# Kernel tuning notes

Hardware: AMD Instinct MI355X
Metric: run time of the kernel (lower is better)

## Reference

```python
import jax, jax.numpy as jnp
import numpy as np

N = 4096        # nodes
D = 512         # in_dim = hidden_dim
E = 131072      # edges (avg degree 32)
K = 3           # aggregate_range
ALPHA = 2.0


def prelu(x, a):
    return jnp.where(x >= 0, x, a * x)


def setup_inputs() -> dict:
    key = jax.random.key(0)
    ks = jax.random.split(key, 8)
    s = 1.0 / np.sqrt(D)  # ~xavier scale
    return {
        "coeffs": jax.random.normal(ks[0], (N, D), jnp.float32),
        "edge_index": jax.random.randint(ks[1], (2, E), 0, N, dtype=jnp.int32),
        "W0": jax.random.normal(ks[2], (D, D), jnp.float32) * s,
        "b0": jnp.zeros((D,), jnp.float32),
        "a0": jnp.full((1,), 0.25, jnp.float32),
        "W1": jax.random.normal(ks[3], (D, D), jnp.float32) * s,  # use_bias=False
        "a1": jnp.full((1,), 0.25, jnp.float32),
        "W2": jax.random.normal(ks[4], (D, D), jnp.float32) * s,
        "a2": jnp.full((1,), 0.25, jnp.float32),
        "Wo": jax.random.normal(ks[5], (1, D), jnp.float32) * s,
        "bo": jnp.zeros((1,), jnp.float32),
    }


def _mlp(coeffs, W0, b0, a0, W1, a1, W2, a2, Wo, bo):
    # Linear+PReLU, then n_hidden_layers x [Linear(no bias)+PReLU+(Dropout: eval, no-op)], then Linear
    x = prelu(coeffs @ W0.T + b0, a0)
    x = prelu(x @ W1.T, a1)
    x = prelu(x @ W2.T, a2)
    return x @ Wo.T + bo  # [N, 1]


def _aggregate_k_hop(edge_index, angles):
    # Faithful to the torch code: enhanced_angles aliases angles, so each hop
    # reads the CURRENT (already enhanced) values:  a <- a + w_k * A_k @ a.
    # Hop 1 uses raw edge list (duplicate edges add twice). Hops >= 2 use
    # np.unique-deduplicated composed paths == boolean adjacency powers.
    src, dst = edge_index[0], edge_index[1]
    a = angles
    a = a + (0.5 ** ALPHA) * jax.ops.segment_sum(a[dst], src, num_segments=N)
    A = jnp.zeros((N, N), jnp.float32).at[src, dst].set(1.0)  # dedup'd boolean adjacency
    Ak = A
    for k_ in range(K - 1):
        Ak = ((Ak @ A) > 0).astype(jnp.float32)  # unique k-hop paths
        a = a + (1.0 / (k_ + 3)) ** ALPHA * (Ak @ a)
    return a


def reference(coeffs, edge_index, W0, b0, a0, W1, a1, W2, a2, Wo, bo):
    angles = _mlp(coeffs, W0, b0, a0, W1, a1, W2, a2, Wo, bo)
    return _aggregate_k_hop(edge_index, angles)
```

## Files before the change

kernel.cpp:

```cpp
#include <hip/hip_runtime.h>

#define N_NODES 4096
#define D_DIM   512
#define E_EDGES 131072
#define NWORDS  128

typedef __bf16 bf16;
typedef __bf16 bf16x4 __attribute__((ext_vector_type(4)));
typedef __bf16 bf16x8 __attribute__((ext_vector_type(8)));
typedef float  f32x4  __attribute__((ext_vector_type(4)));
typedef unsigned int u32;

#define GLOAD_LDS16(gp, lp) \
    __builtin_amdgcn_global_load_lds((const __attribute__((address_space(1))) u32*)(gp), \
                                     (__attribute__((address_space(3))) u32*)(lp), 16, 0, 0)

static const size_t OFF_W0B = 0;
static const size_t OFF_W1B = OFF_W0B + (size_t)D_DIM*D_DIM*2;
static const size_t OFF_W2B = OFF_W1B + (size_t)D_DIM*D_DIM*2;
static const size_t OFF_X0  = OFF_W2B + (size_t)D_DIM*D_DIM*2;
static const size_t OFF_X1  = OFF_X0  + (size_t)N_NODES*D_DIM*2;
static const size_t OFF_X2  = OFF_X1  + (size_t)N_NODES*D_DIM*2;
static const size_t OFF_ANG = OFF_X2  + (size_t)N_NODES*D_DIM*2;
static const size_t OFF_H1  = OFF_ANG + N_NODES*4;
static const size_t OFF_A2V = OFF_H1  + N_NODES*4;
static const size_t OFF_TP  = OFF_A2V + N_NODES*4;
static const size_t OFF_AB  = OFF_TP  + 1024*4;
static const size_t OFF_A2B = OFF_AB  + (size_t)N_NODES*NWORDS*4;
static const size_t OFF_A3B = OFF_A2B + (size_t)N_NODES*NWORDS*4;

__global__ __launch_bounds__(256)
void prep(const float* __restrict__ coeffs, const float* __restrict__ W0,
          const float* __restrict__ W1, const float* __restrict__ W2,
          const float* __restrict__ bo,
          bf16* __restrict__ x0b, bf16* __restrict__ W0b,
          bf16* __restrict__ W1b, bf16* __restrict__ W2b,
          u32* __restrict__ Ab, float* __restrict__ ang, float* __restrict__ h1)
{
    const int bx = blockIdx.x, t = threadIdx.x;
    if (bx < 512) {
        const float* src = coeffs + (size_t)bx * 4096;
        bf16* dst = x0b + (size_t)bx * 4096;
        #pragma unroll
        for (int i = 0; i < 4; ++i) {
            size_t e = (size_t)(i * 256 + t) * 4;
            float4 v = *(const float4*)(src + e);
            bf16x4 o; o.x = (bf16)v.x; o.y = (bf16)v.y; o.z = (bf16)v.z; o.w = (bf16)v.w;
            *(bf16x4*)(dst + e) = o;
        }
    } else if (bx < 704) {
        int cb = bx - 512;
        const float* src = (cb < 64) ? W0 : (cb < 128) ? W1 : W2;
        bf16* dst = (cb < 64) ? W0b : (cb < 128) ? W1b : W2b;
        size_t base = (size_t)(cb & 63) * 4096;
        #pragma unroll
        for (int i = 0; i < 4; ++i) {
            size_t e = base + (size_t)(i * 256 + t) * 4;
            float4 v = *(const float4*)(src + e);
            bf16x4 o; o.x = (bf16)v.x; o.y = (bf16)v.y; o.z = (bf16)v.z; o.w = (bf16)v.w;
            *(bf16x4*)(dst + e) = o;
        }
    } else if (bx < 832) {
        uint4* dst = (uint4*)Ab + (size_t)(bx - 704) * 1024;
        uint4 z = {0u, 0u, 0u, 0u};
        #pragma unroll
        for (int i = 0; i < 4; ++i) dst[i * 256 + t] = z;
    } else {
        float b = bo[0];
        for (int i = t; i < N_NODES; i += 256) { ang[i] = b; h1[i] = 0.f; }
    }
}

template<int MODE>
__global__ __launch_bounds__(256)
void gemm_fused(const bf16* __restrict__ X, const bf16* __restrict__ W,
                bf16* __restrict__ outB,
                const float* __restrict__ bias, const float* __restrict__ slope,
                const float* __restrict__ Wo, float* __restrict__ ang,
                const int* __restrict__ esrc, const int* __restrict__ edst,
                u32* __restrict__ AbOut,
                const u32* __restrict__ P, const u32* __restrict__ Q, u32* __restrict__ BOut)
{
    __shared__ bf16 At[2][64][64];
    __shared__ bf16 Bt[2][64][64];
    __shared__ int  s_cnt[4];
    __shared__ int  s_list[4][256];
    const int bx = blockIdx.x;
    const int t = threadIdx.x;
    const int wave = t >> 6, lane = t & 63;

    if (bx < 512) {
        const int wm = wave >> 1, wn = wave & 1;
        const int quad = lane >> 4, lq = lane & 15;
        const int rowBase = (bx >> 3) * 64;
        const int colBase = (bx & 7) * 64;
        const int c0 = t, c1 = t + 256;
        const int r0 = c0 >> 3, o0 = (c0 & 7) * 8;
        const int r1 = c1 >> 3, o1 = (c1 & 7) * 8;

        f32x4 acc[2][2] = {};
        int cur = 0;

        const bf16* gA0 = X + (size_t)(rowBase + r0) * D_DIM + o0;
        const bf16* gA1 = X + (size_t)(rowBase + r1) * D_DIM + o1;
        const bf16* gB0 = W + (size_t)(colBase + r0) * D_DIM + o0;
        const bf16* gB1 = W + (size_t)(colBase + r1) * D_DIM + o1;
        char* baseA = (char*)&At[0][0][0];
        char* baseB = (char*)&Bt[0][0][0];
        GLOAD_LDS16(gA0, baseA + wave * 1024);
        GLOAD_LDS16(gA1, baseA + 4096 + wave * 1024);
        GLOAD_LDS16(gB0, baseB + wave * 1024);
        GLOAD_LDS16(gB1, baseB + 4096 + wave * 1024);
        for (int k0 = 0; k0 < D_DIM; k0 += 64) {
            __syncthreads();
            if (k0 + 64 < D_DIM) {
                int nb = (cur ^ 1) * 8192;
                GLOAD_LDS16(gA0 + k0 + 64, baseA + nb + wave * 1024);
                GLOAD_LDS16(gA1 + k0 + 64, baseA + nb + 4096 + wave * 1024);
                GLOAD_LDS16(gB0 + k0 + 64, baseB + nb + wave * 1024);
                GLOAD_LDS16(gB1 + k0 + 64, baseB + nb + 4096 + wave * 1024);
            }
            #pragma unroll
            for (int kc = 0; kc < 2; ++kc) {
                bf16x8 af[2], bfr[2];
                #pragma unroll
                for (int tm = 0; tm < 2; ++tm) af[tm]  = *(const bf16x8*)&At[cur][wm * 32 + tm * 16 + lq][kc * 32 + quad * 8];
                #pragma unroll
                for (int tn = 0; tn < 2; ++tn) bfr[tn] = *(const bf16x8*)&Bt[cur][wn * 32 + tn * 16 + lq][kc * 32 + quad * 8];
                #pragma unroll
                for (int tm = 0; tm < 2; ++tm)
                    #pragma unroll
                    for (int tn = 0; tn < 2; ++tn)
                        acc[tm][tn] = __builtin_amdgcn_mfma_f32_16x16x32_bf16(af[tm], bfr[tn], acc[tm][tn], 0, 0, 0);
            }
            cur ^= 1;
        }

        const float a = slope[0];
        if (MODE == 2) {
            float wo[2];
            #pragma unroll
            for (int tn = 0; tn < 2; ++tn) wo[tn] = Wo[colBase + wn * 32 + tn * 16 + lq];
            #pragma unroll
            for (int tm = 0; tm < 2; ++tm) {
                #pragma unroll
                for (int r = 0; r < 4; ++r) {
                    float p = 0.f;
                    #pragma unroll
                    for (int tn = 0; tn < 2; ++tn) {
                        float v = acc[tm][tn][r];
                        v = (v >= 0.f) ? v : a * v;
                        p += v * wo[tn];
                    }
                    #pragma unroll
                    for (int m = 1; m < 16; m <<= 1) p += __shfl_xor(p, m, 64);
                    if (lq == 0)
                        atomicAdd(&ang[rowBase + wm * 32 + tm * 16 + quad * 4 + r], p);
                }
            }
        } else {
            #pragma unroll
            for (int tm = 0; tm < 2; ++tm) {
                #pragma unroll
                for (int tn = 0; tn < 2; ++tn) {
                    int col = colBase + wn * 32 + tn * 16 + lq;
                    float b = (MODE == 0) ? bias[col] : 0.f;
                    #pragma unroll
                    for (int r = 0; r < 4; ++r) {
                        int row = rowBase + wm * 32 + tm * 16 + quad * 4 + r;
                        float v = acc[tm][tn][r] + b;
                        v = (v >= 0.f) ? v : a * v;
                        outB[(size_t)row * D_DIM + col] = (bf16)v;
                    }
                }
            }
        }
    } else if (MODE == 0) {
        int base = (bx - 512) * 256 + t;
        for (int e = base; e < E_EDGES; e += 128 * 256) {
            int r = esrc[e], c = edst[e];
            atomicOr(&AbOut[(size_t)r * NWORDS + (c >> 5)], 1u << (c & 31));
        }
    } else {
        int row = (bx - 512) * 4 + wave;
        if (lane == 0) s_cnt[wave] = 0;
        __syncthreads();
        const u32* prow = P + (size_t)row * NWORDS;
        #pragma unroll
        for (int h = 0; h < 2; ++h) {
            u32 bits = prow[h * 64 + lane];
            int base = (h * 64 + lane) * 32;
            while (bits) {
                int b = __ffs(bits) - 1; bits &= bits - 1;
                int pos = atomicAdd(&s_cnt[wave], 1);
                if (pos < 256) s_list[wave][pos] = base + b;
            }
        }
        __syncthreads();
        int cnt = min(s_cnt[wave], 256);
        u32 acc0 = 0, acc1 = 0;
        int j = 0;
        for (; j + 4 <= cnt; j += 4) {
            int i0 = s_list[wave][j], i1 = s_list[wave][j + 1];
            int i2 = s_list[wave][j + 2], i3 = s_list[wave][j + 3];
            const u32* q0 = Q + (size_t)i0 * NWORDS;
            const u32* q1 = Q + (size_t)i1 * NWORDS;
            const u32* q2 = Q + (size_t)i2 * NWORDS;
            const u32* q3 = Q + (size_t)i3 * NWORDS;
            u32 x0 = q0[lane], x1 = q1[lane], x2 = q2[lane], x3 = q3[lane];
            u32 y0 = q0[64 + lane], y1 = q1[64 + lane], y2 = q2[64 + lane], y3 = q3[64 + lane];
            acc0 |= x0 | x1 | x2 | x3;
            acc1 |= y0 | y1 | y2 | y3;
        }
        for (; j < cnt; ++j) {
            const u32* q = Q + (size_t)s_list[wave][j] * NWORDS;
            acc0 |= q[lane]; acc1 |= q[64 + lane];
        }
        BOut[(size_t)row * NWORDS + lane]      = acc0;
        BOut[(size_t)row * NWORDS + 64 + lane] = acc1;
    }
}

__global__ __launch_bounds__(256)
void hop1_edges(const int* __restrict__ src, const int* __restrict__ dst,
                const float* __restrict__ ang, float* __restrict__ h1)
{
    int e = blockIdx.x * 256 + threadIdx.x;
    if (e < E_EDGES) atomicAdd(&h1[src[e]], 0.25f * ang[dst[e]]);
}

__global__ __launch_bounds__(256)
void bits_matvec2(const u32* __restrict__ A2, const float* __restrict__ ang,
                  const float* __restrict__ h1, float* __restrict__ a2,
                  float* __restrict__ Tpart)
{
    __shared__ float aLds[N_NODES];
    __shared__ float s_red[4];
    const int t = threadIdx.x, wave = t >> 6, lane = t & 63;

    #pragma unroll
    for (int i = 0; i < 4; ++i) {
        int e = (i * 256 + t) * 4;
        float4 va = *(const float4*)(ang + e);
        float4 vh = *(const float4*)(h1 + e);
        float4 o; o.x = va.x + vh.x; o.y = va.y + vh.y; o.z = va.z + vh.z; o.w = va.w + vh.w;
        *(float4*)(aLds + e) = o;
    }
    __syncthreads();

    int row = blockIdx.x * 4 + wave;
    float s = 0.f;
    #pragma unroll
    for (int h = 0; h < 2; ++h) {
        u32 bits = A2[(size_t)row * NWORDS + h * 64 + lane];
        int base = (h * 64 + lane) * 32;
        while (bits) {
            int b = __ffs(bits) - 1;
            bits &= bits - 1;
            s += aLds[base + b];
        }
    }
    #pragma unroll
    for (int off = 32; off > 0; off >>= 1) s += __shfl_down(s, off, 64);
    if (lane == 0) {
        float val = aLds[row] + (1.f / 9.f) * s;
        a2[row] = val;
        s_red[wave] = val;
    }
    __syncthreads();
    if (t == 0)
        Tpart[blockIdx.x] = s_red[0] + s_red[1] + s_red[2] + s_red[3];
}

__global__ __launch_bounds__(256)
void bits_matvec3(const u32* __restrict__ A3, const float* __restrict__ a2,
                  const float* __restrict__ Tpart, float* __restrict__ out)
{
    __shared__ float aLds[N_NODES];
    __shared__ float s_part[4];
    const int t = threadIdx.x, wave = t >> 6, lane = t & 63;

    #pragma unroll
    for (int i = 0; i < 4; ++i) {
        int e = (i * 256 + t) * 4;
        *(float4*)(aLds + e) = *(const float4*)(a2 + e);
    }

    float tsum = 0.f;
    #pragma unroll
    for (int i = 0; i < 4; ++i) tsum += Tpart[i * 256 + t];
    #pragma unroll
    for (int off = 32; off > 0; off >>= 1) tsum += __shfl_down(tsum, off, 64);
    if (lane == 0) s_part[wave] = tsum;
    __syncthreads();
    const float T = s_part[0] + s_part[1] + s_part[2] + s_part[3];

    int row = blockIdx.x * 4 + wave;
    float s = 0.f;
    #pragma unroll
    for (int h = 0; h < 2; ++h) {
        u32 bits = ~A3[(size_t)row * NWORDS + h * 64 + lane];
        int base = (h * 64 + lane) * 32;
        while (bits) {
            int b = __ffs(bits) - 1;
            bits &= bits - 1;
            s += aLds[base + b];
        }
    }
    #pragma unroll
    for (int off = 32; off > 0; off >>= 1) s += __shfl_down(s, off, 64);
    if (lane == 0) out[row] = aLds[row] + (1.f / 16.f) * (T - s);
}

extern "C" void kernel_launch(void* const* d_in, const int* in_sizes, int n_in,
                              void* d_out, int out_size, void* d_ws, size_t ws_size,
                              hipStream_t stream) {
    const float* coeffs = (const float*)d_in[0];
    const int*   edges  = (const int*)d_in[1];
    const float* W0     = (const float*)d_in[2];
    const float* b0     = (const float*)d_in[3];
    const float* pa0    = (const float*)d_in[4];
    const float* W1     = (const float*)d_in[5];
    const float* pa1    = (const float*)d_in[6];
    const float* W2     = (const float*)d_in[7];
    const float* pa2    = (const float*)d_in[8];
    const float* Wo     = (const float*)d_in[9];
    const float* bo     = (const float*)d_in[10];
    float* out = (float*)d_out;

    char* ws = (char*)d_ws;
    bf16*  W0b  = (bf16*)(ws + OFF_W0B);
    bf16*  W1b  = (bf16*)(ws + OFF_W1B);
    bf16*  W2b  = (bf16*)(ws + OFF_W2B);
    bf16*  x0b  = (bf16*)(ws + OFF_X0);
    bf16*  x1b  = (bf16*)(ws + OFF_X1);
    bf16*  x2b  = (bf16*)(ws + OFF_X2);
    float* ang  = (float*)(ws + OFF_ANG);
    float* h1   = (float*)(ws + OFF_H1);
    float* a2v  = (float*)(ws + OFF_A2V);
    float* Tp   = (float*)(ws + OFF_TP);
    u32*   Ab   = (u32*)(ws + OFF_AB);
    u32*   A2b  = (u32*)(ws + OFF_A2B);
    u32*   A3b  = (u32*)(ws + OFF_A3B);

    const int* srcp = edges;
    const int* dstp = edges + E_EDGES;

    prep<<<833, 256, 0, stream>>>(coeffs, W0, W1, W2, bo, x0b, W0b, W1b, W2b, Ab, ang, h1);

    gemm_fused<0><<<640, 256, 0, stream>>>(x0b, W0b, x1b, b0, pa0, nullptr, nullptr,
                                           srcp, dstp, Ab, nullptr, nullptr, nullptr);
    gemm_fused<1><<<1536, 256, 0, stream>>>(x1b, W1b, x2b, nullptr, pa1, nullptr, nullptr,
                                            nullptr, nullptr, nullptr, Ab, Ab, A2b);
    gemm_fused<2><<<1536, 256, 0, stream>>>(x2b, W2b, nullptr, nullptr, pa2, Wo, ang,
                                            nullptr, nullptr, nullptr, Ab, A2b, A3b);

    hop1_edges<<<E_EDGES / 256, 256, 0, stream>>>(srcp, dstp, ang, h1);
    bits_matvec2<<<N_NODES / 4, 256, 0, stream>>>(A2b, ang, h1, a2v, Tp);
    bits_matvec3<<<N_NODES / 4, 256, 0, stream>>>(A3b, a2v, Tp, out);
}
```

Baseline: 142.3 us.

## Fuse three MLP GEMMs into one LDS-resident kernel and overlap bit-OR with hops

Replaces the three separate tiled GEMM launches with one kernel. Each 512-thread block keeps a 16-row activation slab in swizzled LDS across all three layers and streams the weights straight from global memory. The block also converts the fp32 inputs itself, so the bf16 intermediate buffers and their global round trips go away. The boolean adjacency-power row-OR work moves out of the GEMM kernels and into the hop-1 and hop-2 aggregation kernels, which cuts the launch count. In exchange, the 16-row tiles give poor weight reuse, since every block rereads all weights from L2. The A² and A³ products now also sit serially on the aggregation chain instead of overlapping with the GEMMs.

```diff
diff --git a/kernel.cpp b/kernel.cpp
--- a/kernel.cpp
+++ b/kernel.cpp
@@ -4,6 +4,7 @@
 #define D_DIM   512
 #define E_EDGES 131072
 #define NWORDS  128
+#define MLP_BLOCKS 256
 
 typedef __bf16 bf16;
 typedef __bf16 bf16x4 __attribute__((ext_vector_type(4)));
@@ -11,17 +12,10 @@
 typedef float  f32x4  __attribute__((ext_vector_type(4)));
 typedef unsigned int u32;
 
-#define GLOAD_LDS16(gp, lp) \
-    __builtin_amdgcn_global_load_lds((const __attribute__((address_space(1))) u32*)(gp), \
-                                     (__attribute__((address_space(3))) u32*)(lp), 16, 0, 0)
-
 static const size_t OFF_W0B = 0;
 static const size_t OFF_W1B = OFF_W0B + (size_t)D_DIM*D_DIM*2;
 static const size_t OFF_W2B = OFF_W1B + (size_t)D_DIM*D_DIM*2;
-static const size_t OFF_X0  = OFF_W2B + (size_t)D_DIM*D_DIM*2;
-static const size_t OFF_X1  = OFF_X0  + (size_t)N_NODES*D_DIM*2;
-static const size_t OFF_X2  = OFF_X1  + (size_t)N_NODES*D_DIM*2;
-static const size_t OFF_ANG = OFF_X2  + (size_t)N_NODES*D_DIM*2;
+static const size_t OFF_ANG = OFF_W2B + (size_t)D_DIM*D_DIM*2;
 static const size_t OFF_H1  = OFF_ANG + N_NODES*4;
 static const size_t OFF_A2V = OFF_H1  + N_NODES*4;
 static const size_t OFF_TP  = OFF_A2V + N_NODES*4;
@@ -29,30 +23,24 @@
 static const size_t OFF_A2B = OFF_AB  + (size_t)N_NODES*NWORDS*4;
 static const size_t OFF_A3B = OFF_A2B + (size_t)N_NODES*NWORDS*4;
 
+__device__ __forceinline__ bf16x8 cvt8(float4 lo, float4 hi) {
+    bf16x8 r;
+    r[0] = (bf16)lo.x; r[1] = (bf16)lo.y; r[2] = (bf16)lo.z; r[3] = (bf16)lo.w;
+    r[4] = (bf16)hi.x; r[5] = (bf16)hi.y; r[6] = (bf16)hi.z; r[7] = (bf16)hi.w;
+    return r;
+}
+
 __global__ __launch_bounds__(256)
-void prep(const float* __restrict__ coeffs, const float* __restrict__ W0,
-          const float* __restrict__ W1, const float* __restrict__ W2,
-          const float* __restrict__ bo,
-          bf16* __restrict__ x0b, bf16* __restrict__ W0b,
-          bf16* __restrict__ W1b, bf16* __restrict__ W2b,
-          u32* __restrict__ Ab, float* __restrict__ ang, float* __restrict__ h1)
+void prep(const float* __restrict__ W0, const float* __restrict__ W1,
+          const float* __restrict__ W2,
+          bf16* __restrict__ W0b, bf16* __restrict__ W1b, bf16* __restrict__ W2b,
+          u32* __restrict__ Ab, float* __restrict__ h1)
 {
     const int bx = blockIdx.x, t = threadIdx.x;
-    if (bx < 512) {
-        const float* src = coeffs + (size_t)bx * 4096;
-        bf16* dst = x0b + (size_t)bx * 4096;
-        #pragma unroll
-        for (int i = 0; i < 4; ++i) {
-            size_t e = (size_t)(i * 256 + t) * 4;
-            float4 v = *(const float4*)(src + e);
-            bf16x4 o; o.x = (bf16)v.x; o.y = (bf16)v.y; o.z = (bf16)v.z; o.w = (bf16)v.w;
-            *(bf16x4*)(dst + e) = o;
-        }
-    } else if (bx < 704) {
-        int cb = bx - 512;
-        const float* src = (cb < 64) ? W0 : (cb < 128) ? W1 : W2;
-        bf16* dst = (cb < 64) ? W0b : (cb < 128) ? W1b : W2b;
-        size_t base = (size_t)(cb & 63) * 4096;
+    if (bx < 192) {
+        const float* src = (bx < 64) ? W0 : (bx < 128) ? W1 : W2;
+        bf16* dst = (bx < 64) ? W0b : (bx < 128) ? W1b : W2b;
+        size_t base = (size_t)(bx & 63) * 4096;
         #pragma unroll
         for (int i = 0; i < 4; ++i) {
             size_t e = base + (size_t)(i * 256 + t) * 4;
@@ -60,216 +48,242 @@
             bf16x4 o; o.x = (bf16)v.x; o.y = (bf16)v.y; o.z = (bf16)v.z; o.w = (bf16)v.w;
             *(bf16x4*)(dst + e) = o;
         }
-    } else if (bx < 832) {
-        uint4* dst = (uint4*)Ab + (size_t)(bx - 704) * 1024;
+    } else if (bx < 320) {
+        uint4* dst = (uint4*)Ab + (size_t)(bx - 192) * 1024;
         uint4 z = {0u, 0u, 0u, 0u};
         #pragma unroll
         for (int i = 0; i < 4; ++i) dst[i * 256 + t] = z;
     } else {
-        float b = bo[0];
-        for (int i = t; i < N_NODES; i += 256) { ang[i] = b; h1[i] = 0.f; }
-    }
-}
-
-template<int MODE>
-__global__ __launch_bounds__(256)
-void gemm_fused(const bf16* __restrict__ X, const bf16* __restrict__ W,
-                bf16* __restrict__ outB,
-                const float* __restrict__ bias, const float* __restrict__ slope,
-                const float* __restrict__ Wo, float* __restrict__ ang,
-                const int* __restrict__ esrc, const int* __restrict__ edst,
-                u32* __restrict__ AbOut,
-                const u32* __restrict__ P, const u32* __restrict__ Q, u32* __restrict__ BOut)
-{
-    __shared__ bf16 At[2][64][64];
-    __shared__ bf16 Bt[2][64][64];
-    __shared__ int  s_cnt[4];
-    __shared__ int  s_list[4][256];
-    const int bx = blockIdx.x;
-    const int t = threadIdx.x;
-    const int wave = t >> 6, lane = t & 63;
-
-    if (bx < 512) {
-        const int wm = wave >> 1, wn = wave & 1;
+        for (int i = t; i < N_NODES; i += 256) h1[i] = 0.f;
+    }
+}
+
+__device__ __forceinline__ void gemm16x64(const bf16 (*xin)[512], const bf16* __restrict__ Wl,
+                                          int col0, int lq, int quad, f32x4 acc[4])
+{
+    #pragma unroll
+    for (int ks = 0; ks < 16; ++ks) {
+        bf16x8 a = *(const bf16x8*)&xin[lq][(((ks * 4 + quad) ^ (lq & 7)) << 3)];
+        #pragma unroll
+        for (int f = 0; f < 4; ++f) {
+            bf16x8 b = *(const bf16x8*)(Wl + (size_t)(col0 + f * 16 + lq) * 512 + ks * 32 + quad * 8);
+            acc[f] = __builtin_amdgcn_mfma_f32_16x16x32_bf16(a, b, acc[f], 0, 0, 0);
+        }
+    }
+}
+
+__device__ __forceinline__ void store_act(bf16 (*xout)[512], const f32x4 acc[4],
+                                          int col0, int lq, int quad,
+                                          const float* __restrict__ bias, float sl)
+{
+    #pragma unroll
+    for (int f = 0; f < 4; ++f) {
+        int col = col0 + f * 16 + lq;
+        float bv = bias ? bias[col] : 0.f;
+        int c = col >> 3, e = col & 7;
+        #pragma unroll
+        for (int r = 0; r < 4; ++r) {
+            int row = quad * 4 + r;
+            float v = acc[f][r] + bv;
+            v = (v >= 0.f) ? v : sl * v;
+            xout[row][((c ^ (row & 7)) << 3) + e] = (bf16)v;
+        }
+    }
+}
+
+__global__ __launch_bounds__(512)
+void mlp_fused(const float* __restrict__ coeffs,
+               const bf16* __restrict__ W0b, const bf16* __restrict__ W1b,
+               const bf16* __restrict__ W2b,
+               const float* __restrict__ b0, const float* __restrict__ pa0,
+               const float* __restrict__ pa1, const float* __restrict__ pa2,
+               const float* __restrict__ Wo, const float* __restrict__ bo,
+               float* __restrict__ ang,
+               const int* __restrict__ esrc, const int* __restrict__ edst,
+               u32* __restrict__ AbOut)
+{
+    __shared__ bf16 xa[16][512];
+    __shared__ bf16 xb[16][512];
+    __shared__ float s_ang[8][16];
+    const int bx = blockIdx.x, t = threadIdx.x;
+
+    if (bx < MLP_BLOCKS) {
+        const int wave = t >> 6, lane = t & 63;
         const int quad = lane >> 4, lq = lane & 15;
-        const int rowBase = (bx >> 3) * 64;
-        const int colBase = (bx & 7) * 64;
-        const int c0 = t, c1 = t + 256;
-        const int r0 = c0 >> 3, o0 = (c0 & 7) * 8;
-        const int r1 = c1 >> 3, o1 = (c1 & 7) * 8;
-
-        f32x4 acc[2][2] = {};
-        int cur = 0;
-
-        const bf16* gA0 = X + (size_t)(rowBase + r0) * D_DIM + o0;
-        const bf16* gA1 = X + (size_t)(rowBase + r1) * D_DIM + o1;
-        const bf16* gB0 = W + (size_t)(colBase + r0) * D_DIM + o0;
-        const bf16* gB1 = W + (size_t)(colBase + r1) * D_DIM + o1;
-        char* baseA = (char*)&At[0][0][0];
-        char* baseB = (char*)&Bt[0][0][0];
-        GLOAD_LDS16(gA0, baseA + wave * 1024);
-        GLOAD_LDS16(gA1, baseA + 4096 + wave * 1024);
-        GLOAD_LDS16(gB0, baseB + wave * 1024);
-        GLOAD_LDS16(gB1, baseB + 4096 + wave * 1024);
-        for (int k0 = 0; k0 < D_DIM; k0 += 64) {
-            __syncthreads();
-            if (k0 + 64 < D_DIM) {
-                int nb = (cur ^ 1) * 8192;
-                GLOAD_LDS16(gA0 + k0 + 64, baseA + nb + wave * 1024);
-                GLOAD_LDS16(gA1 + k0 + 64, baseA + nb + 4096 + wave * 1024);
-                GLOAD_LDS16(gB0 + k0 + 64, baseB + nb + wave * 1024);
-                GLOAD_LDS16(gB1 + k0 + 64, baseB + nb + 4096 + wave * 1024);
+        const int rb = bx * 16;
+        const int col0 = wave * 64;
+
+        {
+            int r = t >> 5;
+            int kc = (t & 31) * 16;
+            const float* src = coeffs + (size_t)(rb + r) * 512 + kc;
+            float4 v0 = *(const float4*)(src);
+            float4 v1 = *(const float4*)(src + 4);
+            float4 v2 = *(const float4*)(src + 8);
+            float4 v3 = *(const float4*)(src + 12);
+            int c0 = kc >> 3;
+            *(bf16x8*)&xa[r][((c0 ^ (r & 7)) << 3)]       = cvt8(v0, v1);
+            *(bf16x8*)&xa[r][(((c0 + 1) ^ (r & 7)) << 3)] = cvt8(v2, v3);
+        }
+        __syncthreads();
+
+        {
+            f32x4 acc[4] = {};
+            gemm16x64(xa, W0b, col0, lq, quad, acc);
+            store_act(xb, acc, col0, lq, quad, b0, pa0[0]);
+        }
+        __syncthreads();
+        {
+            f32x4 acc[4] = {};
+            gemm16x64(xb, W1b, col0, lq, quad, acc);
+            store_act(xa, acc, col0, lq, quad, nullptr, pa1[0]);
+        }
+        __syncthreads();
+        {
+            f32x4 acc[4] = {};
+            gemm16x64(xa, W2b, col0, lq, quad, acc);
+            const float sl = pa2[0];
+            float wo[4];
+            #pragma unroll
+            for (int f = 0; f < 4; ++f) wo[f] = Wo[col0 + f * 16 + lq];
+            #pragma unroll
+            for (int r = 0; r < 4; ++r) {
+                float p = 0.f;
+                #pragma unroll
+                for (int f = 0; f < 4; ++f) {
+                    float v = acc[f][r];
+                    v = (v >= 0.f) ? v : sl * v;
+                    p += v * wo[f];
+                }
+                #pragma unroll
+                for (int m = 1; m < 16; m <<= 1) p += __shfl_xor(p, m, 64);
+                if (lq == 0) s_ang[wave][quad * 4 + r] = p;
             }
+        }
+        __syncthreads();
+        if (t < 16) {
+            float s = bo[0];
             #pragma unroll
-            for (int kc = 0; kc < 2; ++kc) {
-                bf16x8 af[2], bfr[2];
-                #pragma unroll
-                for (int tm = 0; tm < 2; ++tm) af[tm]  = *(const bf16x8*)&At[cur][wm * 32 + tm * 16 + lq][kc * 32 + quad * 8];
-                #pragma unroll
-                for (int tn = 0; tn < 2; ++tn) bfr[tn] = *(const bf16x8*)&Bt[cur][wn * 32 + tn * 16 + lq][kc * 32 + quad * 8];
-                #pragma unroll
-                for (int tm = 0; tm < 2; ++tm)
-                    #pragma unroll
-                    for (int tn = 0; tn < 2; ++tn)
-                        acc[tm][tn] = __builtin_amdgcn_mfma_f32_16x16x32_bf16(af[tm], bfr[tn], acc[tm][tn], 0, 0, 0);
-            }
-            cur ^= 1;
-        }
-
-        const float a = slope[0];
-        if (MODE == 2) {
-            float wo[2];
-            #pragma unroll
-            for (int tn = 0; tn < 2; ++tn) wo[tn] = Wo[colBase + wn * 32 + tn * 16 + lq];
-            #pragma unroll
-            for (int tm = 0; tm < 2; ++tm) {
-                #pragma unroll
-                for (int r = 0; r < 4; ++r) {
-                    float p = 0.f;
-                    #pragma unroll
-                    for (int tn = 0; tn < 2; ++tn) {
-                        float v = acc[tm][tn][r];
-                        v = (v >= 0.f) ? v : a * v;
-                        p += v * wo[tn];
-                    }
-                    #pragma unroll
-                    for (int m = 1; m < 16; m <<= 1) p += __shfl_xor(p, m, 64);
-                    if (lq == 0)
-                        atomicAdd(&ang[rowBase + wm * 32 + tm * 16 + quad * 4 + r], p);
-                }
-            }
-        } else {
-            #pragma unroll
-            for (int tm = 0; tm < 2; ++tm) {
-                #pragma unroll
-                for (int tn = 0; tn < 2; ++tn) {
-                    int col = colBase + wn * 32 + tn * 16 + lq;
-                    float b = (MODE == 0) ? bias[col] : 0.f;
-                    #pragma unroll
-                    for (int r = 0; r < 4; ++r) {
-                        int row = rowBase + wm * 32 + tm * 16 + quad * 4 + r;
-                        float v = acc[tm][tn][r] + b;
-                        v = (v >= 0.f) ? v : a * v;
-                        outB[(size_t)row * D_DIM + col] = (bf16)v;
-                    }
-                }
-            }
-        }
-    } else if (MODE == 0) {
-        int base = (bx - 512) * 256 + t;
-        for (int e = base; e < E_EDGES; e += 128 * 256) {
+            for (int w2 = 0; w2 < 8; ++w2) s += s_ang[w2][t];
+            ang[rb + t] = s;
+        }
+    } else {
+        int base = (bx - MLP_BLOCKS) * 512 + t;
+        for (int e = base; e < E_EDGES; e += 128 * 512) {
             int r = esrc[e], c = edst[e];
             atomicOr(&AbOut[(size_t)r * NWORDS + (c >> 5)], 1u << (c & 31));
         }
+    }
+}
+
+__device__ __forceinline__ void row_or(int row, int wave, int lane,
+                                       int* s_cnt, int (*s_list)[256],
+                                       const u32* __restrict__ P, const u32* __restrict__ Q,
+                                       u32* __restrict__ BOut)
+{
+    if (lane == 0) s_cnt[wave] = 0;
+    __syncthreads();
+    const u32* prow = P + (size_t)row * NWORDS;
+    #pragma unroll
+    for (int h = 0; h < 2; ++h) {
+        u32 bits = prow[h * 64 + lane];
+        int base = (h * 64 + lane) * 32;
+        while (bits) {
+            int b = __ffs(bits) - 1; bits &= bits - 1;
+            int pos = atomicAdd(&s_cnt[wave], 1);
+            if (pos < 256) s_list[wave][pos] = base + b;
+        }
+    }
+    __syncthreads();
+    int cnt = min(s_cnt[wave], 256);
+    u32 acc0 = 0, acc1 = 0;
+    int j = 0;
+    for (; j + 4 <= cnt; j += 4) {
+        int i0 = s_list[wave][j], i1 = s_list[wave][j + 1];
+        int i2 = s_list[wave][j + 2], i3 = s_list[wave][j + 3];
+        const u32* q0 = Q + (size_t)i0 * NWORDS;
+        const u32* q1 = Q + (size_t)i1 * NWORDS;
+        const u32* q2 = Q + (size_t)i2 * NWORDS;
+        const u32* q3 = Q + (size_t)i3 * NWORDS;
+        u32 x0 = q0[lane], x1 = q1[lane], x2 = q2[lane], x3 = q3[lane];
+        u32 y0 = q0[64 + lane], y1 = q1[64 + lane], y2 = q2[64 + lane], y3 = q3[64 + lane];
+        acc0 |= x0 | x1 | x2 | x3;
+        acc1 |= y0 | y1 | y2 | y3;
+    }
+    for (; j < cnt; ++j) {
+        const u32* q = Q + (size_t)s_list[wave][j] * NWORDS;
+        acc0 |= q[lane]; acc1 |= q[64 + lane];
+    }
+    BOut[(size_t)row * NWORDS + lane]      = acc0;
+    BOut[(size_t)row * NWORDS + 64 + lane] = acc1;
+}
+
+__global__ __launch_bounds__(256)
+void hop1_rowor(const int* __restrict__ src, const int* __restrict__ dst,
+                const float* __restrict__ ang, float* __restrict__ h1,
+                const u32* __restrict__ P, const u32* __restrict__ Q, u32* __restrict__ BOut)
+{
+    __shared__ int s_cnt[4];
+    __shared__ int s_list[4][256];
+    const int bx = blockIdx.x, t = threadIdx.x;
+    const int wave = t >> 6, lane = t & 63;
+    if (bx < 512) {
+        int e = bx * 256 + t;
+        atomicAdd(&h1[src[e]], 0.25f * ang[dst[e]]);
     } else {
-        int row = (bx - 512) * 4 + wave;
-        if (lane == 0) s_cnt[wave] = 0;
-        __syncthreads();
-        const u32* prow = P + (size_t)row * NWORDS;
+        row_or((bx - 512) * 4 + wave, wave, lane, s_cnt, s_list, P, Q, BOut);
+    }
+}
+
+__global__ __launch_bounds__(256)
+void bmv2_rowor(const u32* __restrict__ A2, const float* __restrict__ ang,
+                const float* __restrict__ h1, float* __restrict__ a2,
+                float* __restrict__ Tpart,
+                const u32* __restrict__ P, const u32* __restrict__ Q, u32* __restrict__ BOut)
+{
+    __shared__ float aLds[N_NODES];
+    __shared__ float s_red[4];
+    __shared__ int s_cnt[4];
+    __shared__ int s_list[4][256];
+    const int bx = blockIdx.x, t = threadIdx.x;
+    const int wave = t >> 6, lane = t & 63;
+
+    if (bx < 1024) {
+        #pragma unroll
+        for (int i = 0; i < 4; ++i) {
+            int e = (i * 256 + t) * 4;
+            float4 va = *(const float4*)(ang + e);
+            float4 vh = *(const float4*)(h1 + e);
+            float4 o; o.x = va.x + vh.x; o.y = va.y + vh.y; o.z = va.z + vh.z; o.w = va.w + vh.w;
+            *(float4*)(aLds + e) = o;
+        }
+        __syncthreads();
+
+        int row = bx * 4 + wave;
+        float s = 0.f;
         #pragma unroll
         for (int h = 0; h < 2; ++h) {
-            u32 bits = prow[h * 64 + lane];
+            u32 bits = A2[(size_t)row * NWORDS + h * 64 + lane];
             int base = (h * 64 + lane) * 32;
             while (bits) {
-                int b = __ffs(bits) - 1; bits &= bits - 1;
-                int pos = atomicAdd(&s_cnt[wave], 1);
-                if (pos < 256) s_list[wave][pos] = base + b;
+                int b = __ffs(bits) - 1;
+                bits &= bits - 1;
+                s += aLds[base + b];
             }
         }
-        __syncthreads();
-        int cnt = min(s_cnt[wave], 256);
-        u32 acc0 = 0, acc1 = 0;
-        int j = 0;
-        for (; j + 4 <= cnt; j += 4) {
-            int i0 = s_list[wave][j], i1 = s_list[wave][j + 1];
-            int i2 = s_list[wave][j + 2], i3 = s_list[wave][j + 3];
-            const u32* q0 = Q + (size_t)i0 * NWORDS;
-            const u32* q1 = Q + (size_t)i1 * NWORDS;
-            const u32* q2 = Q + (size_t)i2 * NWORDS;
-            const u32* q3 = Q + (size_t)i3 * NWORDS;
-            u32 x0 = q0[lane], x1 = q1[lane], x2 = q2[lane], x3 = q3[lane];
-            u32 y0 = q0[64 + lane], y1 = q1[64 + lane], y2 = q2[64 + lane], y3 = q3[64 + lane];
-            acc0 |= x0 | x1 | x2 | x3;
-            acc1 |= y0 | y1 | y2 | y3;
-        }
-        for (; j < cnt; ++j) {
-            const u32* q = Q + (size_t)s_list[wave][j] * NWORDS;
-            acc0 |= q[lane]; acc1 |= q[64 + lane];
-        }
-        BOut[(size_t)row * NWORDS + lane]      = acc0;
-        BOut[(size_t)row * NWORDS + 64 + lane] = acc1;
-    }
-}
-
-__global__ __launch_bounds__(256)
-void hop1_edges(const int* __restrict__ src, const int* __restrict__ dst,
-                const float* __restrict__ ang, float* __restrict__ h1)
-{
-    int e = blockIdx.x * 256 + threadIdx.x;
-    if (e < E_EDGES) atomicAdd(&h1[src[e]], 0.25f * ang[dst[e]]);
-}
-
-__global__ __launch_bounds__(256)
-void bits_matvec2(const u32* __restrict__ A2, const float* __restrict__ ang,
-                  const float* __restrict__ h1, float* __restrict__ a2,
-                  float* __restrict__ Tpart)
-{
-    __shared__ float aLds[N_NODES];
-    __shared__ float s_red[4];
-    const int t = threadIdx.x, wave = t >> 6, lane = t & 63;
-
-    #pragma unroll
-    for (int i = 0; i < 4; ++i) {
-        int e = (i * 256 + t) * 4;
-        float4 va = *(const float4*)(ang + e);
-        float4 vh = *(const float4*)(h1 + e);
-        float4 o; o.x = va.x + vh.x; o.y = va.y + vh.y; o.z = va.z + vh.z; o.w = va.w + vh.w;
-        *(float4*)(aLds + e) = o;
-    }
-    __syncthreads();
-
-    int row = blockIdx.x * 4 + wave;
-    float s = 0.f;
-    #pragma unroll
-    for (int h = 0; h < 2; ++h) {
-        u32 bits = A2[(size_t)row * NWORDS + h * 64 + lane];
-        int base = (h * 64 + lane) * 32;
-        while (bits) {
-            int b = __ffs(bits) - 1;
-            bits &= bits - 1;
-            s += aLds[base + b];
-        }
-    }
-    #pragma unroll
-    for (int off = 32; off > 0; off >>= 1) s += __shfl_down(s, off, 64);
-    if (lane == 0) {
-        float val = aLds[row] + (1.f / 9.f) * s;
-        a2[row] = val;
-        s_red[wave] = val;
-    }
-    __syncthreads();
-    if (t == 0)
-        Tpart[blockIdx.x] = s_red[0] + s_red[1] + s_red[2] + s_red[3];
+        #pragma unroll
+        for (int off = 32; off > 0; off >>= 1) s += __shfl_down(s, off, 64);
+        if (lane == 0) {
+            float val = aLds[row] + (1.f / 9.f) * s;
+            a2[row] = val;
+            s_red[wave] = val;
+        }
+        __syncthreads();
+        if (t == 0)
+            Tpart[bx] = s_red[0] + s_red[1] + s_red[2] + s_red[3];
+    } else {
+        row_or((bx - 1024) * 4 + wave, wave, lane, s_cnt, s_list, P, Q, BOut);
+    }
 }
 
 __global__ __launch_bounds__(256)
@@ -332,9 +346,6 @@
     bf16*  W0b  = (bf16*)(ws + OFF_W0B);
     bf16*  W1b  = (bf16*)(ws + OFF_W1B);
     bf16*  W2b  = (bf16*)(ws + OFF_W2B);
-    bf16*  x0b  = (bf16*)(ws + OFF_X0);
-    bf16*  x1b  = (bf16*)(ws + OFF_X1);
-    bf16*  x2b  = (bf16*)(ws + OFF_X2);
     float* ang  = (float*)(ws + OFF_ANG);
     float* h1   = (float*)(ws + OFF_H1);
     float* a2v  = (float*)(ws + OFF_A2V);
@@ -346,16 +357,14 @@
     const int* srcp = edges;
     const int* dstp = edges + E_EDGES;
 
-    prep<<<833, 256, 0, stream>>>(coeffs, W0, W1, W2, bo, x0b, W0b, W1b, W2b, Ab, ang, h1);
-
-    gemm_fused<0><<<640, 256, 0, stream>>>(x0b, W0b, x1b, b0, pa0, nullptr, nullptr,
-                                           srcp, dstp, Ab, nullptr, nullptr, nullptr);
-    gemm_fused<1><<<1536, 256, 0, stream>>>(x1b, W1b, x2b, nullptr, pa1, nullptr, nullptr,
-                                            nullptr, nullptr, nullptr, Ab, Ab, A2b);
-    gemm_fused<2><<<1536, 256, 0, stream>>>(x2b, W2b, nullptr, nullptr, pa2, Wo, ang,
-                                            nullptr, nullptr, nullptr, Ab, A2b, A3b);
-
-    hop1_edges<<<E_EDGES / 256, 256, 0, stream>>>(srcp, dstp, ang, h1);
-    bits_matvec2<<<N_NODES / 4, 256, 0, stream>>>(A2b, ang, h1, a2v, Tp);
-    bits_matvec3<<<N_NODES / 4, 256, 0, stream>>>(A3b, a2v, Tp, out);
-}
+    prep<<<321, 256, 0, stream>>>(W0, W1, W2, W0b, W1b, W2b, Ab, h1);
+
+    mlp_fused<<<MLP_BLOCKS + 128, 512, 0, stream>>>(coeffs, W0b, W1b, W2b, b0, pa0, pa1, pa2,
+                                                    Wo, bo, ang, srcp, dstp, Ab);
+
+    hop1_rowor<<<1536, 256, 0, stream>>>(srcp, dstp, ang, h1, Ab, Ab, A2b);
+
+    bmv2_rowor<<<2048, 256, 0, stream>>>(A2b, ang, h1, a2v, Tp, Ab, A2b, A3b);
+
+    bits_matvec3<<<1024, 256, 0, stream>>>(A3b, a2v, Tp, out);
+}
```

After: 158.5 us. +11.4%, slower.
